# Optimization experiments

Measured on AMD Instinct MI355X. Metric: run time of the kernel, lower is better.

The kernel has to match this reference:

```python
import jax, jax.numpy as jnp
import numpy as np

BT, N = 4, 2048
FIN, FOUT = 512, 128          # GGE in/out; FOUT == PPI output (GAGA constraint)
PIN, POUT = 256, 128          # PPIGE in/out
HEAD = 4
K = POUT // HEAD              # per-head dim = 32
NEG_SLOPE = 0.2
MASK_VAL = -1e30


def setup_inputs() -> dict:
    key = jax.random.key(0)
    ks = jax.random.split(key, 24)
    s = 0.05
    inp = {}
    inp["a"] = jax.random.normal(ks[0], (BT, FIN), jnp.float32)
    inp["bio_a"] = jax.random.normal(ks[1], (BT, N, PIN), jnp.float32)
    inp["A"] = jax.random.randint(ks[2], (BT, N, N), 0, 2, jnp.int32)
    inp["b"] = jax.random.normal(ks[3], (BT, FIN), jnp.float32)
    inp["bio_b"] = jax.random.normal(ks[4], (BT, N, PIN), jnp.float32)
    inp["B"] = jax.random.randint(ks[5], (BT, N, N), 0, 2, jnp.int32)
    # PPIGE_GAT params (shared across both graph branches)
    inp["initW"] = jax.random.normal(ks[6], (POUT, PIN), jnp.float32) * s
    inp["initb"] = jnp.zeros((POUT,), jnp.float32)
    inp["projW"] = jax.random.normal(ks[7], (POUT, POUT), jnp.float32) * s  # no bias
    inp["attw"] = jax.random.normal(ks[8], (HEAD, 2 * K), jnp.float32) * s  # per-head [2k]->1
    inp["attb"] = jnp.zeros((HEAD,), jnp.float32)
    # GGE params
    inp["ggeW1"] = jax.random.normal(ks[9], (128, FIN), jnp.float32) * s
    inp["ggeb1"] = jnp.zeros((128,), jnp.float32)
    inp["ggeW2"] = jax.random.normal(ks[10], (FOUT, 128), jnp.float32) * s
    inp["ggeb2"] = jnp.zeros((FOUT,), jnp.float32)
    # LED params (hidden = FOUT)
    inp["convW"] = jax.random.normal(ks[11], (2 * FOUT, 2 * FOUT), jnp.float32) * s  # k=1 conv
    inp["convb"] = jnp.zeros((2 * FOUT,), jnp.float32)
    inp["ledW1"] = jax.random.normal(ks[12], (FOUT, 4 * FOUT), jnp.float32) * s
    inp["ledb1"] = jnp.zeros((FOUT,), jnp.float32)
    inp["ledW2"] = jax.random.normal(ks[13], (2, FOUT), jnp.float32) * s
    inp["ledb2"] = jnp.zeros((2,), jnp.float32)
    return inp


def _gat_layer(x, adj_mask, projW, attw, attb):
    # x: [B,N,POUT]; adj_mask: [B,N,N] bool
    Bt, n, _ = x.shape
    xh = (x @ projW.T).reshape(Bt, n, HEAD, K).transpose(0, 2, 1, 3)  # [B,h,N,k]
    # score(i,j) = leaky_relu(w1.x_i + w2.x_j + b)  (equivalent to Linear on concat)
    s1 = jnp.einsum('bhnk,hk->bhn', xh, attw[:, :K])
    s2 = jnp.einsum('bhnk,hk->bhn', xh, attw[:, K:])
    scores = jax.nn.leaky_relu(
        s1[..., :, None] + s2[..., None, :] + attb[None, :, None, None], NEG_SLOPE)
    scores = jnp.where(adj_mask[:, None], scores, MASK_VAL)
    att = jax.nn.softmax(scores, axis=-1)                     # [B,h,N,N]
    out = jax.nn.relu(att @ xh)                               # [B,h,N,k]
    return out.transpose(0, 2, 1, 3).reshape(Bt, n, HEAD * K)


def _ppige(bio, adj, initW, initb, projW, attw, attb):
    x = bio @ initW.T + initb
    return _gat_layer(x, adj > 0, projW, attw, attb) + x      # residual; dropout=eval


def _gge(a, W1, b1, W2, b2):
    h = jax.nn.relu(a @ W1.T + b1)
    return jax.nn.relu(h @ W2.T + b2)


def _gaga(G, h):
    # G: [B,N,D], h: [B,D]
    att = jax.nn.softmax(jnp.einsum('bnd,bd->bn', G, h), axis=-1)
    return jnp.einsum('bnd,bn->bd', G, att)


def _led(ea, eb, convW, convb, W1, b1, W2, b2):
    # pointwise conv over the length-2 stack [ea, eb], then maxpool over length
    cnn = jnp.maximum(ea @ convW.T + convb, eb @ convW.T + convb)  # [B,2D]
    x = jax.nn.relu(jnp.concatenate([cnn, ea - eb], axis=1) @ W1.T + b1)
    return x @ W2.T + b2


def reference(a, bio_a, A, b, bio_b, B,
              initW, initb, projW, attw, attb,
              ggeW1, ggeb1, ggeW2, ggeb2,
              convW, convb, ledW1, ledb1, ledW2, ledb2):
    G_a = _ppige(bio_a, A, initW, initb, projW, attw, attb)
    G_b = _ppige(bio_b, B, initW, initb, projW, attw, attb)
    h_a = _gge(a, ggeW1, ggeb1, ggeW2, ggeb2)
    h_b = _gge(b, ggeW1, ggeb1, ggeW2, ggeb2)
    e_a = jnp.concatenate([h_a, _gaga(G_a, h_a)], axis=-1)
    e_b = jnp.concatenate([h_b, _gaga(G_b, h_b)], axis=-1)
    logits = _led(e_a, e_b, convW, convb, ledW1, ledb1, ledW2, ledb2)
    return jax.nn.log_softmax(logits, axis=-1)
```

## Files before the change

kernel.cpp:

```cpp
#include <hip/hip_runtime.h>
#include <hip/hip_bf16.h>
#include <math.h>

#define NN 2048
#define NEG 0.2f
#define LOG2E 1.44269504f

typedef short bf16x8 __attribute__((ext_vector_type(8)));
typedef float f32x16 __attribute__((ext_vector_type(16)));

__device__ __forceinline__ float dot4(float4 a, float4 b) {
  return a.x * b.x + a.y * b.y + a.z * b.z + a.w * b.w;
}

__device__ __forceinline__ unsigned short bfbits(float f) {
  union { __hip_bfloat16 b; unsigned short u; } c;
  c.b = __float2bfloat16(f);
  return c.u;
}

__global__ __launch_bounds__(256) void k1_init(const float* __restrict__ bioA,
                                               const float* __restrict__ bioB,
                                               const float* __restrict__ W,
                                               const float* __restrict__ bias,
                                               float* __restrict__ xout) {
  __shared__ float As[32][36];
  __shared__ float Ws[32][132];
  const int t = threadIdx.x;
  const int m0 = blockIdx.x * 32;
  const float* A = (m0 < 8192) ? bioA : bioB;
  const int arow0 = (m0 < 8192) ? m0 : (m0 - 8192);
  const int og = t & 31, ig = t >> 5;
  float acc[4][4] = {};
  for (int kt = 0; kt < 256; kt += 32) {
    __syncthreads();
    {
      const int r = t >> 3, kq = t & 7;
      const float4 v = *(const float4*)&A[(arow0 + r) * 256 + kt + kq * 4];
      As[kq * 4 + 0][r] = v.x; As[kq * 4 + 1][r] = v.y;
      As[kq * 4 + 2][r] = v.z; As[kq * 4 + 3][r] = v.w;
    }
#pragma unroll
    for (int u = 0; u < 4; ++u) {
      const int f = u * 256 + t;
      const int o = f >> 3, kq = f & 7;
      const float4 v = *(const float4*)&W[o * 256 + kt + kq * 4];
      Ws[kq * 4 + 0][o] = v.x; Ws[kq * 4 + 1][o] = v.y;
      Ws[kq * 4 + 2][o] = v.z; Ws[kq * 4 + 3][o] = v.w;
    }
    __syncthreads();
#pragma unroll
    for (int kk = 0; kk < 32; ++kk) {
      const float4 a4 = *(const float4*)&As[kk][ig * 4];
      const float4 w4 = *(const float4*)&Ws[kk][og * 4];
      const float av[4] = {a4.x, a4.y, a4.z, a4.w};
      const float wv[4] = {w4.x, w4.y, w4.z, w4.w};
#pragma unroll
      for (int ii = 0; ii < 4; ++ii)
#pragma unroll
        for (int jj = 0; jj < 4; ++jj) acc[ii][jj] += av[ii] * wv[jj];
    }
  }
  const float4 b4 = *(const float4*)&bias[og * 4];
#pragma unroll
  for (int ii = 0; ii < 4; ++ii) {
    const int row = m0 + ig * 4 + ii;
    float4 o4;
    o4.x = acc[ii][0] + b4.x; o4.y = acc[ii][1] + b4.y;
    o4.z = acc[ii][2] + b4.z; o4.w = acc[ii][3] + b4.w;
    *(float4*)&xout[row * 128 + og * 4] = o4;
  }
}

__global__ __launch_bounds__(256) void k2_proj(const float* __restrict__ x,
                                               const float* __restrict__ W,
                                               const float* __restrict__ attw,
                                               unsigned short* __restrict__ xhT2,
                                               float* __restrict__ s1,
                                               float* __restrict__ s2) {
  __shared__ float As[32][36];
  __shared__ float Ws[32][132];
  const int t = threadIdx.x;
  const int m0 = blockIdx.x * 32;
  const int og = t & 31, ig = t >> 5;
  float acc[4][4] = {};
  for (int kt = 0; kt < 128; kt += 32) {
    __syncthreads();
    {
      const int r = t >> 3, kq = t & 7;
      const float4 v = *(const float4*)&x[(m0 + r) * 128 + kt + kq * 4];
      As[kq * 4 + 0][r] = v.x; As[kq * 4 + 1][r] = v.y;
      As[kq * 4 + 2][r] = v.z; As[kq * 4 + 3][r] = v.w;
    }
#pragma unroll
    for (int u = 0; u < 4; ++u) {
      const int f = u * 256 + t;
      const int o = f >> 3, kq = f & 7;
      const float4 v = *(const float4*)&W[o * 128 + kt + kq * 4];
      Ws[kq * 4 + 0][o] = v.x; Ws[kq * 4 + 1][o] = v.y;
      Ws[kq * 4 + 2][o] = v.z; Ws[kq * 4 + 3][o] = v.w;
    }
    __syncthreads();
#pragma unroll
    for (int kk = 0; kk < 32; ++kk) {
      const float4 a4 = *(const float4*)&As[kk][ig * 4];
      const float4 w4 = *(const float4*)&Ws[kk][og * 4];
      const float av[4] = {a4.x, a4.y, a4.z, a4.w};
      const float wv[4] = {w4.x, w4.y, w4.z, w4.w};
#pragma unroll
      for (int ii = 0; ii < 4; ++ii)
#pragma unroll
        for (int jj = 0; jj < 4; ++jj) acc[ii][jj] += av[ii] * wv[jj];
    }
  }
  const int h = og >> 3;
  const int k4i = (og & 7) * 4;
  const int g = m0 >> 13;
  const int bb = (m0 >> 11) & 3;
  const int gb = g * 4 + bb;
  const int n0 = (m0 & 2047) + ig * 4;
  const float4 w1 = *(const float4*)&attw[h * 64 + k4i];
  const float4 w2 = *(const float4*)&attw[h * 64 + 32 + k4i];
  float p1[4], p2[4];
#pragma unroll
  for (int ii = 0; ii < 4; ++ii) {
    float4 v;
    v.x = acc[ii][0]; v.y = acc[ii][1]; v.z = acc[ii][2]; v.w = acc[ii][3];
    p1[ii] = dot4(v, w1);
    p2[ii] = dot4(v, w2);
  }
  {
    const int mtile = n0 >> 4, jslot = (n0 >> 3) & 1, j8 = n0 & 7;
    const int base2 = ((((gb * 4 + h) * 128 + mtile) * 2 + jslot) * 32) * 8 + j8;
#pragma unroll
    for (int jj = 0; jj < 4; ++jj) {
      const int kin = k4i + jj;
      ushort4 u;
      u.x = bfbits(acc[0][jj]); u.y = bfbits(acc[1][jj]);
      u.z = bfbits(acc[2][jj]); u.w = bfbits(acc[3][jj]);
      *(ushort4*)&xhT2[base2 + kin * 8] = u;
    }
  }
#pragma unroll
  for (int s = 1; s < 8; s <<= 1) {
#pragma unroll
    for (int ii = 0; ii < 4; ++ii) {
      p1[ii] += __shfl_xor(p1[ii], s);
      p2[ii] += __shfl_xor(p2[ii], s);
    }
  }
  if ((og & 7) == 0) {
#pragma unroll
    for (int ii = 0; ii < 4; ++ii) {
      s1[(gb * 4 + h) * NN + n0 + ii] = p1[ii];
      s2[(gb * 4 + h) * NN + n0 + ii] = p2[ii];
    }
  }
}

__global__ __launch_bounds__(512) void k3_attn(const unsigned short* __restrict__ xhT2,
                                               const float* __restrict__ s1w,
                                               const float* __restrict__ s2w,
                                               const int* __restrict__ adjA,
                                               const int* __restrict__ adjB,
                                               const float* __restrict__ attb,
                                               const float* __restrict__ x,
                                               float* __restrict__ G) {
  __shared__ unsigned int adjL[32][66];
  __shared__ float s2L[4][2048];
  __shared__ float accR[4][16][65];
  __shared__ float denR[4][2][32];
  const int t = threadIdx.x;
  const int wave = t >> 6, lane = t & 63;
  const int blk = blockIdx.x;
  const int g = blk >> 8, b = (blk >> 6) & 3;
  const int i0 = (blk & 63) * 32;
  const int gb = g * 4 + b;
  const int* adj = (g ? adjB : adjA) + (b * NN + i0) * NN;
  {
    const float* s2g = s2w + gb * 4 * NN;
    float* s2f = &s2L[0][0];
#pragma unroll
    for (int u = 0; u < 4; ++u) {
      const int idx = u * 2048 + t * 4;
      float4 v = *(const float4*)&s2g[idx];
      v.x *= LOG2E; v.y *= LOG2E; v.z *= LOG2E; v.w *= LOG2E;
      *(float4*)&s2f[idx] = v;
    }
  }
#pragma unroll
  for (int r4 = 0; r4 < 4; ++r4) {
    const int r = wave * 4 + r4;
    const int* arow = adj + r * NN;
#pragma unroll 4
    for (int w = 0; w < 32; ++w) {
      const int av = arow[w * 64 + lane];
      const unsigned long long m = __ballot(av > 0);
      if (lane < 2) adjL[r][2 * w + lane] = (unsigned int)(m >> (32 * lane));
    }
  }
  __syncthreads();

  const int h = wave & 3;
  const int jhalf = wave >> 2;
  const int jlo = jhalf * 1024;
  const int i = lane & 31;
  const int jslot = lane >> 5;
  const float sc1v = (s1w[(gb * 4 + h) * NN + i0 + i] + attb[h]) * LOG2E;
  const unsigned short* bbase = xhT2 + (gb * 4 + h) * 65536 + jhalf * 64 * 512
                                + jslot * 256 + i * 8;
  f32x16 acc = {0.f, 0.f, 0.f, 0.f, 0.f, 0.f, 0.f, 0.f,
                0.f, 0.f, 0.f, 0.f, 0.f, 0.f, 0.f, 0.f};
  float den4[4] = {0.f, 0.f, 0.f, 0.f};
  bf16x8 buf[4];
#pragma unroll
  for (int q = 0; q < 4; ++q) buf[q] = *(const bf16x8*)&bbase[512 * q];
  for (int mb = 0; mb < 64; mb += 4) {
#pragma unroll
    for (int q = 0; q < 4; ++q) {
      const int m = mb + q;
      const bf16x8 bnext = *(const bf16x8*)&bbase[512 * (m + 4)];
      const int j0 = jlo + 16 * m + jslot * 8;
      const unsigned int wbits = adjL[i][(jlo + 16 * m) >> 5];
      const unsigned int bits8 = wbits >> ((m & 1) * 16 + jslot * 8);
      const float4 s2a = *(const float4*)&s2L[h][j0];
      const float4 s2b = *(const float4*)&s2L[h][j0 + 4];
      const float sv[8] = {s2a.x, s2a.y, s2a.z, s2a.w, s2b.x, s2b.y, s2b.z, s2b.w};
      union { bf16x8 v; unsigned short u[8]; } af;
      float dsum = 0.f;
#pragma unroll
      for (int e = 0; e < 8; ++e) {
        float s = sc1v + sv[e];
        s = fmaxf(s, NEG * s);
        float pe = __builtin_amdgcn_exp2f(s);
        pe = ((bits8 >> e) & 1u) ? pe : 0.f;
        af.u[e] = bfbits(pe);
        dsum += pe;
      }
      den4[q] += dsum;
      acc = __builtin_amdgcn_mfma_f32_32x32x16_bf16(af.v, buf[q], acc, 0, 0, 0);
      buf[q] = bnext;
    }
  }
  float den = (den4[0] + den4[1]) + (den4[2] + den4[3]);
  den += __shfl_xor(den, 32);
  if (lane < 32) denR[h][jhalf][lane] = den;
  if (jhalf == 1) {
#pragma unroll
    for (int r = 0; r < 16; ++r) accR[h][r][lane] = acc[r];
  }
  __syncthreads();
  if (jhalf == 0) {
#pragma unroll
    for (int r = 0; r < 16; ++r) {
      const int row = (r & 3) + 8 * (r >> 2) + 4 * jslot;
      const float dinv = 1.f / (denR[h][0][row] + denR[h][1][row]);
      const int off = (gb * NN + i0 + row) * 128 + h * 32 + i;
      const float av = acc[r] + accR[h][r][lane];
      G[off] = fmaxf(av * dinv, 0.f) + x[off];
    }
  }
}

__global__ __launch_bounds__(256) void k4h_gge(const float* __restrict__ a_in,
                                               const float* __restrict__ b_in,
                                               const float* __restrict__ ggeW1,
                                               const float* __restrict__ ggeb1,
                                               const float* __restrict__ ggeW2,
                                               const float* __restrict__ ggeb2,
                                               float* __restrict__ hvbuf,
                                               float* __restrict__ e) {
  __shared__ float inL[512];
  __shared__ float h1L[128];
  const int t = threadIdx.x;
  const int wave = t >> 6, lane = t & 63;
  const int g = blockIdx.x >> 2, b = blockIdx.x & 3;
  const int gb2 = g * 4 + b;
  const float* inp = (g ? b_in : a_in) + b * 512;
  if (t < 128) *(float4*)&inL[t * 4] = *(const float4*)&inp[t * 4];
  __syncthreads();
  for (int p = 0; p < 16; ++p) {
    const int o0 = p * 8 + wave * 2;
    const float* w0 = &ggeW1[o0 * 512 + lane * 8];
    const float* w1 = &ggeW1[(o0 + 1) * 512 + lane * 8];
    const float4 i0v = *(const float4*)&inL[lane * 8];
    const float4 i1v = *(const float4*)&inL[lane * 8 + 4];
    float s0 = dot4(*(const float4*)&w0[0], i0v) + dot4(*(const float4*)&w0[4], i1v);
    float s1v = dot4(*(const float4*)&w1[0], i0v) + dot4(*(const float4*)&w1[4], i1v);
#pragma unroll
    for (int s = 1; s < 64; s <<= 1) { s0 += __shfl_xor(s0, s); s1v += __shfl_xor(s1v, s); }
    if (lane == 0) {
      h1L[o0] = fmaxf(s0 + ggeb1[o0], 0.f);
      h1L[o0 + 1] = fmaxf(s1v + ggeb1[o0 + 1], 0.f);
    }
  }
  __syncthreads();
  for (int p = 0; p < 16; ++p) {
    const int o0 = p * 8 + wave * 2;
    const float2 w0 = *(const float2*)&ggeW2[o0 * 128 + lane * 2];
    const float2 w1 = *(const float2*)&ggeW2[(o0 + 1) * 128 + lane * 2];
    const float2 hvv = *(const float2*)&h1L[lane * 2];
    float s0 = w0.x * hvv.x + w0.y * hvv.y;
    float s1v = w1.x * hvv.x + w1.y * hvv.y;
#pragma unroll
    for (int s = 1; s < 64; s <<= 1) { s0 += __shfl_xor(s0, s); s1v += __shfl_xor(s1v, s); }
    if (lane == 0) {
      const float v0 = fmaxf(s0 + ggeb2[o0], 0.f);
      const float v1 = fmaxf(s1v + ggeb2[o0 + 1], 0.f);
      hvbuf[gb2 * 128 + o0] = v0;
      hvbuf[gb2 * 128 + o0 + 1] = v1;
      e[gb2 * 256 + o0] = v0;
      e[gb2 * 256 + o0 + 1] = v1;
    }
  }
}

__global__ __launch_bounds__(256) void k4a_logits(const float* __restrict__ G,
                                                  const float* __restrict__ hv,
                                                  float* __restrict__ lg) {
  const int t = threadIdx.x;
  const int wave = t >> 6, lane = t & 63;
  const int gb = blockIdx.x >> 4, chunk = blockIdx.x & 15;
  const float2 hvv = *(const float2*)&hv[gb * 128 + lane * 2];
  const float* Gb = G + gb * NN * 128;
  const int nbase = chunk * 128 + wave * 32;
  for (int q = 0; q < 32; ++q) {
    const int n = nbase + q;
    const float2 gv = *(const float2*)&Gb[n * 128 + lane * 2];
    float part = gv.x * hvv.x + gv.y * hvv.y;
#pragma unroll
    for (int s = 1; s < 64; s <<= 1) part += __shfl_xor(part, s);
    if (lane == 0) lg[gb * NN + n] = part;
  }
}

__global__ __launch_bounds__(256) void k4b_reduce(const float* __restrict__ lg,
                                                  float* __restrict__ mz) {
  __shared__ float red[256];
  const int t = threadIdx.x;
  const int gb = blockIdx.x;
  const float* l = lg + gb * NN;
  float m = -1e30f;
  for (int n = t; n < NN; n += 256) m = fmaxf(m, l[n]);
  red[t] = m; __syncthreads();
#pragma unroll
  for (int s = 128; s > 0; s >>= 1) {
    if (t < s) red[t] = fmaxf(red[t], red[t + s]);
    __syncthreads();
  }
  const float mx = red[0]; __syncthreads();
  float z = 0.f;
  for (int n = t; n < NN; n += 256) z += __expf(l[n] - mx);
  red[t] = z; __syncthreads();
#pragma unroll
  for (int s = 128; s > 0; s >>= 1) {
    if (t < s) red[t] += red[t + s];
    __syncthreads();
  }
  if (t == 0) { mz[gb * 2] = mx; mz[gb * 2 + 1] = red[0]; }
}

__global__ __launch_bounds__(256) void k4c_wsum(const float* __restrict__ G,
                                                const float* __restrict__ lg,
                                                const float* __restrict__ mz,
                                                float* __restrict__ wsum) {
  __shared__ float pL[128];
  __shared__ float red[2][128];
  const int t = threadIdx.x;
  const int gb = blockIdx.x >> 4, chunk = blockIdx.x & 15;
  const float mx = mz[gb * 2];
  if (t < 128) pL[t] = __expf(lg[gb * NN + chunk * 128 + t] - mx);
  __syncthreads();
  const int d = t & 127, half = t >> 7;
  const float* Gb = G + (gb * NN + chunk * 128 + half * 64) * 128;
  float acc = 0.f;
  for (int q = 0; q < 64; ++q) acc += pL[half * 64 + q] * Gb[q * 128 + d];
  red[half][d] = acc;
  __syncthreads();
  if (t < 128) wsum[(gb * 16 + chunk) * 128 + t] = red[0][t] + red[1][t];
}

__global__ __launch_bounds__(128) void k4d_final(const float* __restrict__ wsum,
                                                 const float* __restrict__ mz,
                                                 float* __restrict__ e) {
  const int t = threadIdx.x;
  const int gb = blockIdx.x;
  float s = 0.f;
#pragma unroll
  for (int c = 0; c < 16; ++c) s += wsum[(gb * 16 + c) * 128 + t];
  e[gb * 256 + 128 + t] = s / mz[gb * 2 + 1];
}

__global__ __launch_bounds__(256) void k5_led(const float* __restrict__ e,
                                              const float* __restrict__ convW,
                                              const float* __restrict__ convb,
                                              const float* __restrict__ ledW1,
                                              const float* __restrict__ ledb1,
                                              const float* __restrict__ ledW2,
                                              const float* __restrict__ ledb2,
                                              float* __restrict__ out) {
  __shared__ float eaL[256], ebL[256], uL[512], xL[128], lgL[2];
  const int t = threadIdx.x;
  const int wave = t >> 6, lane = t & 63;
  const int bt = blockIdx.x;
  if (t < 64) {
    *(float4*)&eaL[t * 4] = *(const float4*)&e[bt * 256 + t * 4];
    *(float4*)&ebL[t * 4] = *(const float4*)&e[(4 + bt) * 256 + t * 4];
  }
  __syncthreads();
  uL[256 + t] = eaL[t] - ebL[t];
  const float4 ea4 = *(const float4*)&eaL[lane * 4];
  const float4 eb4 = *(const float4*)&ebL[lane * 4];
  for (int p = 0; p < 32; ++p) {
    const int o0 = p * 8 + wave * 2;
    const float4 w0 = *(const float4*)&convW[o0 * 256 + lane * 4];
    const float4 w1 = *(const float4*)&convW[(o0 + 1) * 256 + lane * 4];
    float sa0 = dot4(w0, ea4), sb0 = dot4(w0, eb4);
    float sa1 = dot4(w1, ea4), sb1 = dot4(w1, eb4);
#pragma unroll
    for (int s = 1; s < 64; s <<= 1) {
      sa0 += __shfl_xor(sa0, s); sb0 += __shfl_xor(sb0, s);
      sa1 += __shfl_xor(sa1, s); sb1 += __shfl_xor(sb1, s);
    }
    if (lane == 0) {
      const float c0 = convb[o0], c1 = convb[o0 + 1];
      uL[o0] = fmaxf(sa0 + c0, sb0 + c0);
      uL[o0 + 1] = fmaxf(sa1 + c1, sb1 + c1);
    }
  }
  __syncthreads();
  for (int p = 0; p < 16; ++p) {
    const int o0 = p * 8 + wave * 2;
    const float* w0 = &ledW1[o0 * 512 + lane * 8];
    const float* w1 = &ledW1[(o0 + 1) * 512 + lane * 8];
    const float4 u0 = *(const float4*)&uL[lane * 8];
    const float4 u1 = *(const float4*)&uL[lane * 8 + 4];
    float s0 = dot4(*(const float4*)&w0[0], u0) + dot4(*(const float4*)&w0[4], u1);
    float s1v = dot4(*(const float4*)&w1[0], u0) + dot4(*(const float4*)&w1[4], u1);
#pragma unroll
    for (int s = 1; s < 64; s <<= 1) { s0 += __shfl_xor(s0, s); s1v += __shfl_xor(s1v, s); }
    if (lane == 0) {
      xL[o0] = fmaxf(s0 + ledb1[o0], 0.f);
      xL[o0 + 1] = fmaxf(s1v + ledb1[o0 + 1], 0.f);
    }
  }
  __syncthreads();
  if (wave < 2) {
    const float2 w = *(const float2*)&ledW2[wave * 128 + lane * 2];
    const float2 xv = *(const float2*)&xL[lane * 2];
    float s0 = w.x * xv.x + w.y * xv.y;
#pragma unroll
    for (int s = 1; s < 64; s <<= 1) s0 += __shfl_xor(s0, s);
    if (lane == 0) lgL[wave] = s0 + ledb2[wave];
  }
  __syncthreads();
  if (t == 0) {
    const float l0 = lgL[0], l1 = lgL[1];
    const float m = fmaxf(l0, l1);
    const float za = __expf(l0 - m) + __expf(l1 - m);
    const float lz = __logf(za);
    out[bt * 2 + 0] = l0 - m - lz;
    out[bt * 2 + 1] = l1 - m - lz;
  }
}

extern "C" void kernel_launch(void* const* d_in, const int* in_sizes, int n_in,
                              void* d_out, int out_size, void* d_ws, size_t ws_size,
                              hipStream_t stream) {
  (void)in_sizes; (void)n_in; (void)out_size; (void)ws_size;
  const float* a     = (const float*)d_in[0];
  const float* bioA  = (const float*)d_in[1];
  const int*   A     = (const int*)d_in[2];
  const float* b     = (const float*)d_in[3];
  const float* bioB  = (const float*)d_in[4];
  const int*   B     = (const int*)d_in[5];
  const float* initW = (const float*)d_in[6];
  const float* initb = (const float*)d_in[7];
  const float* projW = (const float*)d_in[8];
  const float* attw  = (const float*)d_in[9];
  const float* attb  = (const float*)d_in[10];
  const float* ggeW1 = (const float*)d_in[11];
  const float* ggeb1 = (const float*)d_in[12];
  const float* ggeW2 = (const float*)d_in[13];
  const float* ggeb2 = (const float*)d_in[14];
  const float* convW = (const float*)d_in[15];
  const float* convb = (const float*)d_in[16];
  const float* ledW1 = (const float*)d_in[17];
  const float* ledb1 = (const float*)d_in[18];
  const float* ledW2 = (const float*)d_in[19];
  const float* ledb2 = (const float*)d_in[20];

  float* ws = (float*)d_ws;
  float*          x    = ws;
  unsigned short* xhT2 = (unsigned short*)(ws + 2097152);
  float*          s1   = ws + 3145728;
  float*          s2   = ws + 3211264;
  float*          G    = ws + 3276800;
  float*          lg   = ws + 5373952;
  float*          wsum = ws + 5390336;
  float*          mz   = ws + 5406720;
  float*          hv   = ws + 5406736;
  float*          e    = ws + 5407760;
  float* out = (float*)d_out;

  k1_init<<<512, 256, 0, stream>>>(bioA, bioB, initW, initb, x);
  k2_proj<<<512, 256, 0, stream>>>(x, projW, attw, xhT2, s1, s2);
  k3_attn<<<512, 512, 0, stream>>>(xhT2, s1, s2, A, B, attb, x, G);
  k4h_gge<<<8, 256, 0, stream>>>(a, b, ggeW1, ggeb1, ggeW2, ggeb2, hv, e);
  k4a_logits<<<128, 256, 0, stream>>>(G, hv, lg);
  k4b_reduce<<<8, 256, 0, stream>>>(lg, mz);
  k4c_wsum<<<128, 256, 0, stream>>>(G, lg, mz, wsum);
  k4d_final<<<8, 128, 0, stream>>>(wsum, mz, e);
  k5_led<<<4, 256, 0, stream>>>(e, convW, convb, ledW1, ledb1, ledW2, ledb2, out);
}
```

Measured before the change: 195.7 us.

## Stage attention B fragments through LDS with async global_load_lds ring buffer

The attention kernel now streams each wave's bf16 value fragments into a per-wave 4-slot LDS ring via global_load_lds, using explicit vmcnt waits, instead of holding a 4-deep register prefetch. Shared memory is repacked into one manually laid-out buffer, with the cross-wave accumulator reduction aliasing the adjacency/s2 region and an extra barrier added. The aim is to cut VGPR pressure and overlap loads with exp/MFMA work. It costs about 75 KB of LDS per block, which may limit occupancy, and adds an LDS read per step.

```diff
diff --git a/kernel.cpp b/kernel.cpp
--- a/kernel.cpp
+++ b/kernel.cpp
@@ -17,6 +17,20 @@
   union { __hip_bfloat16 b; unsigned short u; } c;
   c.b = __float2bfloat16(f);
   return c.u;
+}
+
+template <int VM>
+__device__ __forceinline__ void waitv() {
+  if constexpr (VM == 0) asm volatile("s_waitcnt vmcnt(0)" ::: "memory");
+  else if constexpr (VM == 1) asm volatile("s_waitcnt vmcnt(1)" ::: "memory");
+  else if constexpr (VM == 2) asm volatile("s_waitcnt vmcnt(2)" ::: "memory");
+  else asm volatile("s_waitcnt vmcnt(3)" ::: "memory");
+}
+
+__device__ __forceinline__ void stage_frag(const unsigned short* g, char* l) {
+  __builtin_amdgcn_global_load_lds(
+      (const __attribute__((address_space(1))) unsigned int*)g,
+      (__attribute__((address_space(3))) unsigned int*)l, 16, 0, 0);
 }
 
 __global__ __launch_bounds__(256) void k1_init(const float* __restrict__ bioA,
@@ -166,10 +180,13 @@
                                                const float* __restrict__ attb,
                                                const float* __restrict__ x,
                                                float* __restrict__ G) {
-  __shared__ unsigned int adjL[32][66];
-  __shared__ float s2L[4][2048];
-  __shared__ float accR[4][16][65];
-  __shared__ float denR[4][2][32];
+  __shared__ __align__(16) unsigned char smem3[75008];
+  unsigned int* adjL = (unsigned int*)smem3;
+  float* s2L = (float*)(smem3 + 8448);
+  float* denR = (float*)(smem3 + 41216);
+  char* bufs = (char*)(smem3 + 42240);
+  float* accR = (float*)smem3;
+
   const int t = threadIdx.x;
   const int wave = t >> 6, lane = t & 63;
   const int blk = blockIdx.x;
@@ -179,13 +196,12 @@
   const int* adj = (g ? adjB : adjA) + (b * NN + i0) * NN;
   {
     const float* s2g = s2w + gb * 4 * NN;
-    float* s2f = &s2L[0][0];
 #pragma unroll
     for (int u = 0; u < 4; ++u) {
       const int idx = u * 2048 + t * 4;
       float4 v = *(const float4*)&s2g[idx];
       v.x *= LOG2E; v.y *= LOG2E; v.z *= LOG2E; v.w *= LOG2E;
-      *(float4*)&s2f[idx] = v;
+      *(float4*)&s2L[idx] = v;
     }
   }
 #pragma unroll
@@ -196,7 +212,7 @@
     for (int w = 0; w < 32; ++w) {
       const int av = arow[w * 64 + lane];
       const unsigned long long m = __ballot(av > 0);
-      if (lane < 2) adjL[r][2 * w + lane] = (unsigned int)(m >> (32 * lane));
+      if (lane < 2) adjL[r * 66 + 2 * w + lane] = (unsigned int)(m >> (32 * lane));
     }
   }
   __syncthreads();
@@ -207,56 +223,66 @@
   const int i = lane & 31;
   const int jslot = lane >> 5;
   const float sc1v = (s1w[(gb * 4 + h) * NN + i0 + i] + attb[h]) * LOG2E;
-  const unsigned short* bbase = xhT2 + (gb * 4 + h) * 65536 + jhalf * 64 * 512
-                                + jslot * 256 + i * 8;
+  const unsigned short* bbase = xhT2 + (gb * 4 + h) * 65536 + jhalf * 32768 + lane * 8;
+  char* wrb = bufs + wave * 4096;
+  const char* rdb = wrb + lane * 16;
   f32x16 acc = {0.f, 0.f, 0.f, 0.f, 0.f, 0.f, 0.f, 0.f,
                 0.f, 0.f, 0.f, 0.f, 0.f, 0.f, 0.f, 0.f};
-  float den4[4] = {0.f, 0.f, 0.f, 0.f};
-  bf16x8 buf[4];
-#pragma unroll
-  for (int q = 0; q < 4; ++q) buf[q] = *(const bf16x8*)&bbase[512 * q];
-  for (int mb = 0; mb < 64; mb += 4) {
-#pragma unroll
-    for (int q = 0; q < 4; ++q) {
-      const int m = mb + q;
-      const bf16x8 bnext = *(const bf16x8*)&bbase[512 * (m + 4)];
-      const int j0 = jlo + 16 * m + jslot * 8;
-      const unsigned int wbits = adjL[i][(jlo + 16 * m) >> 5];
-      const unsigned int bits8 = wbits >> ((m & 1) * 16 + jslot * 8);
-      const float4 s2a = *(const float4*)&s2L[h][j0];
-      const float4 s2b = *(const float4*)&s2L[h][j0 + 4];
-      const float sv[8] = {s2a.x, s2a.y, s2a.z, s2a.w, s2b.x, s2b.y, s2b.z, s2b.w};
-      union { bf16x8 v; unsigned short u[8]; } af;
-      float dsum = 0.f;
-#pragma unroll
-      for (int e = 0; e < 8; ++e) {
-        float s = sc1v + sv[e];
-        s = fmaxf(s, NEG * s);
-        float pe = __builtin_amdgcn_exp2f(s);
-        pe = ((bits8 >> e) & 1u) ? pe : 0.f;
-        af.u[e] = bfbits(pe);
-        dsum += pe;
-      }
-      den4[q] += dsum;
-      acc = __builtin_amdgcn_mfma_f32_32x32x16_bf16(af.v, buf[q], acc, 0, 0, 0);
-      buf[q] = bnext;
-    }
-  }
-  float den = (den4[0] + den4[1]) + (den4[2] + den4[3]);
+  float den = 0.f;
+  stage_frag(bbase + 0 * 512, wrb + 0 * 1024);
+  stage_frag(bbase + 1 * 512, wrb + 1 * 1024);
+  stage_frag(bbase + 2 * 512, wrb + 2 * 1024);
+
+#define K3_STEP(MM, VM, DOSTAGE)                                              \
+  {                                                                           \
+    if (DOSTAGE)                                                              \
+      stage_frag(bbase + ((MM) + 3) * 512, wrb + (((MM) + 3) & 3) * 1024);    \
+    waitv<VM>();                                                              \
+    const bf16x8 bcur = *(const bf16x8*)(rdb + ((MM) & 3) * 1024);            \
+    const int j0 = jlo + 16 * (MM) + jslot * 8;                               \
+    const unsigned int wbits = adjL[i * 66 + ((jlo + 16 * (MM)) >> 5)];       \
+    const unsigned int bits8 = wbits >> ((((MM) & 1) * 16) + jslot * 8);      \
+    const float4 s2a = *(const float4*)&s2L[h * 2048 + j0];                   \
+    const float4 s2b = *(const float4*)&s2L[h * 2048 + j0 + 4];               \
+    const float sv[8] = {s2a.x, s2a.y, s2a.z, s2a.w,                          \
+                         s2b.x, s2b.y, s2b.z, s2b.w};                         \
+    union { bf16x8 v; unsigned short u[8]; } af;                              \
+    float dsum = 0.f;                                                         \
+    _Pragma("unroll")                                                         \
+    for (int e = 0; e < 8; ++e) {                                             \
+      float s = sc1v + sv[e];                                                 \
+      s = fmaxf(s, NEG * s);                                                  \
+      float pe = __builtin_amdgcn_exp2f(s);                                   \
+      pe = ((bits8 >> e) & 1u) ? pe : 0.f;                                    \
+      af.u[e] = bfbits(pe);                                                   \
+      dsum += pe;                                                             \
+    }                                                                         \
+    den += dsum;                                                              \
+    acc = __builtin_amdgcn_mfma_f32_32x32x16_bf16(af.v, bcur, acc, 0, 0, 0);  \
+  }
+
+#pragma unroll 4
+  for (int m = 0; m <= 60; ++m) K3_STEP(m, 3, true);
+  K3_STEP(61, 2, false);
+  K3_STEP(62, 1, false);
+  K3_STEP(63, 0, false);
+#undef K3_STEP
+
   den += __shfl_xor(den, 32);
-  if (lane < 32) denR[h][jhalf][lane] = den;
+  if (lane < 32) denR[(h * 2 + jhalf) * 32 + lane] = den;
+  __syncthreads();
   if (jhalf == 1) {
 #pragma unroll
-    for (int r = 0; r < 16; ++r) accR[h][r][lane] = acc[r];
+    for (int r = 0; r < 16; ++r) accR[(h * 16 + r) * 65 + lane] = acc[r];
   }
   __syncthreads();
   if (jhalf == 0) {
 #pragma unroll
     for (int r = 0; r < 16; ++r) {
       const int row = (r & 3) + 8 * (r >> 2) + 4 * jslot;
-      const float dinv = 1.f / (denR[h][0][row] + denR[h][1][row]);
+      const float dinv = 1.f / (denR[(h * 2 + 0) * 32 + row] + denR[(h * 2 + 1) * 32 + row]);
       const int off = (gb * NN + i0 + row) * 128 + h * 32 + i;
-      const float av = acc[r] + accR[h][r][lane];
+      const float av = acc[r] + accR[(h * 16 + r) * 65 + lane];
       G[off] = fmaxf(av * dinv, 0.f) + x[off];
     }
   }
```

After: 205.8 us. +5.2%, slower.
